# Performance work log

Measured on AMD Instinct MI355X. Metric: run time of the kernel, lower is better.

Reference implementation:

```python
import jax, jax.numpy as jnp
import numpy as np

V, E, H, B, S, T = 32000, 32, 128, 128, 512, 16


def _gru_cell(x, h, w_ih, w_hh, b_ih, b_hh):
    # PyTorch GRU cell semantics.  x: [B, in], h: [B, H]
    gi = x @ w_ih.T + b_ih              # [B, 3H]
    gh = h @ w_hh.T + b_hh              # [B, 3H]
    i_r, i_z, i_n = jnp.split(gi, 3, axis=-1)
    h_r, h_z, h_n = jnp.split(gh, 3, axis=-1)
    r = jax.nn.sigmoid(i_r + h_r)
    z = jax.nn.sigmoid(i_z + h_z)
    n = jnp.tanh(i_n + r * h_n)
    return (1.0 - z) * n + z * h


def setup_inputs() -> dict:
    key = jax.random.key(0)
    ks = jax.random.split(key, 24)
    Hh = H // 2  # encoder hidden per direction = 64
    u = lambda k, shp, fan: jax.random.uniform(k, shp, jnp.float32, -1.0, 1.0) / np.sqrt(fan)
    inp = {
        'inputs': jax.random.randint(ks[0], (B, S), 0, V),
        'targets': jax.random.randint(ks[1], (B, T), 0, V),
        'emb': jax.random.normal(ks[2], (V, E), jnp.float32),
        # encoder forward direction
        'W_ih_f': u(ks[3], (3 * Hh, E), Hh), 'W_hh_f': u(ks[4], (3 * Hh, Hh), Hh),
        'b_ih_f': u(ks[5], (3 * Hh,), Hh), 'b_hh_f': u(ks[6], (3 * Hh,), Hh),
        # encoder backward direction
        'W_ih_b': u(ks[7], (3 * Hh, E), Hh), 'W_hh_b': u(ks[8], (3 * Hh, Hh), Hh),
        'b_ih_b': u(ks[9], (3 * Hh,), Hh), 'b_hh_b': u(ks[10], (3 * Hh,), Hh),
        # sGate linears
        'W1': u(ks[11], (H, H), H), 'b1': u(ks[12], (H,), H),
        'W2': u(ks[13], (H, H), H), 'b2': u(ks[14], (H,), H),
        # decoder GRU (input E + H = 160, hidden H)
        'W_ih_d': u(ks[15], (3 * H, E + H), H), 'W_hh_d': u(ks[16], (3 * H, H), H),
        'b_ih_d': u(ks[17], (3 * H,), H), 'b_hh_d': u(ks[18], (3 * H,), H),
        # decoder2vocab
        'W_out': u(ks[19], (V, H), H), 'b_out': u(ks[20], (V,), H),
    }
    return inp


def reference(inputs, targets, emb, W_ih_f, W_hh_f, b_ih_f, b_hh_f,
              W_ih_b, W_hh_b, b_ih_b, b_hh_b, W1, b1, W2, b2,
              W_ih_d, W_hh_d, b_ih_d, b_hh_d, W_out, b_out):
    Hh = H // 2
    # ---- encode ----
    embeds = emb[inputs]                       # [B, S, E]
    xs = embeds.transpose(1, 0, 2)             # [S, B, E] time-major
    h0 = jnp.zeros((inputs.shape[0], Hh), jnp.float32)

    def fwd_step(h, x):
        h = _gru_cell(x, h, W_ih_f, W_hh_f, b_ih_f, b_hh_f)
        return h, h

    def bwd_step(h, x):
        h = _gru_cell(x, h, W_ih_b, W_hh_b, b_ih_b, b_hh_b)
        return h, h

    h_f, outs_f = jax.lax.scan(fwd_step, h0, xs)
    h_b, outs_b = jax.lax.scan(bwd_step, h0, xs[::-1])
    outs_b = outs_b[::-1]
    outputs = jnp.concatenate([outs_f, outs_b], axis=-1).transpose(1, 0, 2)  # [B, S, H]
    sn = jnp.concatenate([h_f, h_b], axis=-1)[:, None, :]                    # [B, 1, H]
    sGate = jax.nn.sigmoid(outputs @ W1.T + b1 + sn @ W2.T + b2)
    enc_outs = outputs * sGate                                               # [B, S, H]

    # ---- attention decode (teacher forcing) ----
    h_dec0 = sn[:, 0, :]                       # [B, H]
    words = targets[:, :-1].T                  # [T-1, B]

    def dec_step(h, w):
        e = emb[w]                                                  # [B, E]
        alpha = jax.nn.softmax(jnp.einsum('bd,bsd->bs', h, enc_outs))
        c_t = jnp.einsum('bs,bsd->bd', alpha, enc_outs)             # [B, H]
        h = _gru_cell(jnp.concatenate([c_t, e], axis=-1), h,
                      W_ih_d, W_hh_d, b_ih_d, b_hh_d)
        return h, h @ W_out.T + b_out

    _, logits = jax.lax.scan(dec_step, h_dec0, words)  # [T-1, B, V]
    return logits.transpose(1, 0, 2)                   # [B, T-1, V]
```

## Files before the change

kernel.cpp:

```cpp
#include <hip/hip_runtime.h>
#include <hip/hip_bf16.h>


typedef unsigned short u16;
typedef unsigned int u32;
typedef __attribute__((ext_vector_type(8))) short short8;
typedef __attribute__((ext_vector_type(4))) float f32x4;

#define V_ 32000
#define E_ 32
#define H_ 128
#define B_ 128
#define S_ 512
#define TDEC 15

__device__ __forceinline__ float bfu(u32 u) {
    union { u32 i; float f; } v; v.i = u << 16; return v.f;
}
__device__ __forceinline__ u16 f2bf(float f) {
    union { float f; u32 i; } v; v.f = f;
    u32 x = v.i;
    u32 r = (x + 0x7fffu + ((x >> 16) & 1u)) >> 16;
    return (u16)r;
}
__device__ __forceinline__ void bf8_to_f(const uint4 p, float* f) {
    f[0] = bfu(p.x & 0xffffu); f[1] = bfu(p.x >> 16);
    f[2] = bfu(p.y & 0xffffu); f[3] = bfu(p.y >> 16);
    f[4] = bfu(p.z & 0xffffu); f[5] = bfu(p.z >> 16);
    f[6] = bfu(p.w & 0xffffu); f[7] = bfu(p.w >> 16);
}
__device__ __forceinline__ float sigm_fast(float x) { return 1.f / (1.f + __expf(-x)); }
__device__ __forceinline__ float tanh_fast(float x) {
    const float t = __expf(2.f * x);
    return (t - 1.f) / (t + 1.f);
}

__global__ __launch_bounds__(384) void gi_kernel(
    const int* __restrict__ inputs, const float* __restrict__ emb,
    const float* __restrict__ Wih_f, const float* __restrict__ bih_f,
    const float* __restrict__ bhh_f,
    const float* __restrict__ Wih_b, const float* __restrict__ bih_b,
    const float* __restrict__ bhh_b,
    float* __restrict__ gi)
{
    const int b  = blockIdx.x >> 3;
    const int s0 = (blockIdx.x & 7) << 6;
    const int tid = threadIdx.x;

    __shared__ float xs[64][E_];
    __shared__ int idx[64];
    if (tid < 64) idx[tid] = inputs[b * S_ + s0 + tid];
    __syncthreads();
    for (int i = tid; i < 64 * E_; i += 384) {
        xs[i >> 5][i & 31] = emb[(unsigned)idx[i >> 5] * E_ + (i & 31)];
    }
    __syncthreads();

    const int dir = (tid >= 192) ? 1 : 0;
    const int j = tid - dir * 192;
    const float* Wih = dir ? Wih_b : Wih_f;
    const float* bih = dir ? bih_b : bih_f;
    const float* bhh = dir ? bhh_b : bhh_f;

    float w[E_];
    #pragma unroll
    for (int k = 0; k < E_; k += 4)
        *(float4*)(w + k) = *(const float4*)(Wih + j * E_ + k);
    const float c = bih[j] + (j < 128 ? bhh[j] : 0.f);

    float* gout = gi + (((size_t)(dir * B_ + b)) * S_ + s0) * 192 + j;
    for (int r = 0; r < 64; r++) {
        const float4* xr = (const float4*)xs[r];
        float a0 = 0.f, a1 = 0.f, a2 = 0.f, a3 = 0.f;
        #pragma unroll
        for (int q = 0; q < E_ / 4; q++) {
            const float4 x = xr[q];
            a0 += x.x * w[4 * q + 0]; a1 += x.y * w[4 * q + 1];
            a2 += x.z * w[4 * q + 2]; a3 += x.w * w[4 * q + 3];
        }
        gout[(size_t)r * 192] = ((a0 + a1) + (a2 + a3)) + c;
    }
}

__global__ __launch_bounds__(192, 1) void encoder_kernel(
    const float* __restrict__ gi,
    const float* __restrict__ Whh_f, const float* __restrict__ bhh_f,
    const float* __restrict__ Whh_b, const float* __restrict__ bhh_b,
    u16* __restrict__ outputs, float* __restrict__ sn)
{
    const int tid = threadIdx.x;
    const int g = tid >> 6;
    const int j = tid & 63;
    const int b = blockIdx.x & 127;
    const int dir = blockIdx.x >> 7;

    const float* Whh = dir ? Whh_b : Whh_f;
    const float* bhh = dir ? bhh_b : bhh_f;

    f32x4 wv[16];
    {
        const f32x4* wr = (const f32x4*)(Whh + (g * 64 + j) * 64);
        #pragma unroll
        for (int k = 0; k < 16; k++) wv[k] = wr[k];
    }
    const float badd = (g == 2) ? bhh[128 + j] : 0.f;

    __shared__ __attribute__((aligned(16))) float hs[64];
    __shared__ float sg[4 * 64];
    if (tid < 64) hs[tid] = 0.f;
    float hmine = 0.f;

    const float* gp = gi + ((size_t)(dir * B_ + b)) * S_ * 192 + g * 64 + j;
    u16* orow = outputs + ((size_t)b * S_) * H_ + (dir << 6) + j;

    const int st = dir ? -1 : 1;
    int oc = dir ? (S_ - 1) : 0;

    float pa = gp[(long)oc * 192];
    float pb = gp[(long)(oc + st) * 192];

#define ENC_STEP(PCUR)                                                         \
    {                                                                          \
        __syncthreads();                  \
        f32x4 acc = {0.f, 0.f, 0.f, 0.f};                                      \
        _Pragma("unroll")                                                      \
        for (int q = 0; q < 16; q++)                                           \
            acc += *(const f32x4*)(hs + 4 * q) * wv[q];                        \
        const float d = (acc[0] + acc[1]) + (acc[2] + acc[3]);                 \
        if (g == 2) { sg[128 + j] = d + badd; sg[192 + j] = PCUR; }            \
        else        { sg[g * 64 + j] = d + PCUR; }                             \
        PCUR = gp[(long)(oc + 2 * st) * 192];           \
        __syncthreads();                                         \
        if (g == 0) {                                                          \
            const float r = sigm_fast(sg[j]);                                  \
            const float z = sigm_fast(sg[64 + j]);                             \
            const float n = tanh_fast(sg[192 + j] + r * sg[128 + j]);          \
            const float hn = n + z * (hmine - n);                              \
            hmine = hn;                                                        \
            hs[j] = hn;                                                        \
            orow[(long)oc * H_] = f2bf(hn);                                    \
        }                                                                      \
        oc += st;                                                              \
    }

    for (int s = 0; s < S_; s += 2) {
        ENC_STEP(pa)
        ENC_STEP(pb)
    }
#undef ENC_STEP

    if (g == 0) sn[(b << 7) + (dir << 6) + j] = hmine;
}

__global__ __launch_bounds__(128) void t2_kernel(
    const float* __restrict__ sn, const float* __restrict__ W2,
    const float* __restrict__ b2, float* __restrict__ t2)
{
    const int b = blockIdx.x, h = threadIdx.x;
    __shared__ float s_[H_];
    s_[h] = sn[b * H_ + h];
    __syncthreads();
    const float4* wr = (const float4*)(W2 + h * H_);
    float a0 = 0.f, a1 = 0.f, a2 = 0.f, a3 = 0.f;
    #pragma unroll 4
    for (int k = 0; k < H_ / 4; k++) {
        const float4 p = wr[k];
        a0 += s_[4 * k + 0] * p.x; a1 += s_[4 * k + 1] * p.y;
        a2 += s_[4 * k + 2] * p.z; a3 += s_[4 * k + 3] * p.w;
    }
    t2[b * H_ + h] = ((a0 + a1) + (a2 + a3)) + b2[h];
}

__global__ __launch_bounds__(256) void cvt_bf16_kernel(
    const float* __restrict__ src, u16* __restrict__ dst)
{
    const int i = (blockIdx.x * 256 + threadIdx.x) * 4;
    const float4 p = *(const float4*)(src + i);
    ushort4 q;
    q.x = f2bf(p.x); q.y = f2bf(p.y); q.z = f2bf(p.z); q.w = f2bf(p.w);
    *(ushort4*)(dst + i) = q;
}

__global__ __launch_bounds__(256) void gate_mfma_kernel(
    const u16* __restrict__ outputs, const u16* __restrict__ W1b,
    const float* __restrict__ b1, const float* __restrict__ t2,
    u16* __restrict__ enc)
{
    const int l = threadIdx.x & 63;
    const int w = threadIdx.x >> 6;
    const int tile_m = blockIdx.x * 64 + w * 16;
    const int row_a = tile_m + (l & 15);
    const int kb = (l >> 4) * 8;
    const int b = blockIdx.x >> 3;

    f32x4 acc[8] = {};
    #pragma unroll
    for (int kk = 0; kk < 4; kk++) {
        const int k0 = kk * 32 + kb;
        const short8 af = *(const short8*)(outputs + row_a * H_ + k0);
        #pragma unroll
        for (int i = 0; i < 8; i++) {
            const int n = i * 16 + (l & 15);
            const short8 bv = *(const short8*)(W1b + n * H_ + k0);
            acc[i] = __builtin_amdgcn_mfma_f32_16x16x32_bf16(af, bv, acc[i], 0, 0, 0);
        }
    }

    const int m_base = tile_m + (l >> 4) * 4;
    #pragma unroll
    for (int i = 0; i < 8; i++) {
        const int n = i * 16 + (l & 15);
        const float bias = b1[n] + t2[b * H_ + n];
        #pragma unroll
        for (int r = 0; r < 4; r++) {
            const int m = m_base + r;
            const float g = sigm_fast(acc[i][r] + bias);
            const float o = bfu(outputs[m * H_ + n]);
            enc[m * H_ + n] = f2bf(o * g);
        }
    }
}

__global__ __launch_bounds__(512, 1) void decoder_kernel(
    const int* __restrict__ targets, const float* __restrict__ emb,
    const float* __restrict__ Wihd, const float* __restrict__ Whhd,
    const float* __restrict__ bihd, const float* __restrict__ bhhd,
    const u16* __restrict__ enc, const float* __restrict__ sn,
    u16* __restrict__ h_all)
{
    const int b = blockIdx.x;
    const int tid = threadIdx.x;
    const int lane = tid & 63;
    const int wid = tid >> 6;

    __shared__ __attribute__((aligned(16))) u16 enc_lds[S_ * H_];
    __shared__ __attribute__((aligned(16))) float xh[288];
    __shared__ float sc[S_];
    __shared__ float redm[8], reds[8];
    __shared__ __attribute__((aligned(16))) float cpart[32][H_];
    __shared__ float gf[256];
    __shared__ float gin[128], ghn[128];

    const u16* encb = enc + b * S_ * H_;

    {
        const int c = tid & 15;
        const int sb = tid >> 4;
        #pragma unroll
        for (int i = 0; i < 16; i++) {
            const int s = i * 32 + sb;
            const uint4 p = *(const uint4*)(encb + s * H_ + c * 8);
            *(uint4*)(enc_lds + s * H_ + ((c ^ (s & 15)) * 8)) = p;
        }
    }
    if (tid < H_) xh[160 + tid] = sn[b * H_ + tid];
    __syncthreads();

    for (int t = 0; t < TDEC; t++) {
        const int word = targets[b * 16 + t];

        float d;
        {
            const int s = tid;
            const int sx = s & 15;
            float a0 = 0.f, a1 = 0.f, a2 = 0.f, a3 = 0.f;
            #pragma unroll
            for (int c = 0; c < 16; c++) {
                const uint4 p = *(const uint4*)(enc_lds + s * H_ + ((c ^ sx) * 8));
                float f[8]; bf8_to_f(p, f);
                const f32x4 h0 = *(const f32x4*)(xh + 160 + c * 8);
                const f32x4 h1 = *(const f32x4*)(xh + 160 + c * 8 + 4);
                a0 += h0[0] * f[0]; a1 += h0[1] * f[1];
                a2 += h0[2] * f[2]; a3 += h0[3] * f[3];
                a0 += h1[0] * f[4]; a1 += h1[1] * f[5];
                a2 += h1[2] * f[6]; a3 += h1[3] * f[7];
            }
            d = (a0 + a1) + (a2 + a3);
        }

        float m = d;
        #pragma unroll
        for (int off = 32; off > 0; off >>= 1) m = fmaxf(m, __shfl_xor(m, off));
        if (lane == 0) redm[wid] = m;
        __syncthreads();
        float bm = redm[0];
        #pragma unroll
        for (int i = 1; i < 8; i++) bm = fmaxf(bm, redm[i]);
        const float e = __expf(d - bm);
        float ssum = e;
        #pragma unroll
        for (int off = 32; off > 0; off >>= 1) ssum += __shfl_xor(ssum, off);
        if (lane == 0) reds[wid] = ssum;
        __syncthreads();
        float tot = reds[0];
        #pragma unroll
        for (int i = 1; i < 8; i++) tot += reds[i];
        sc[tid] = e * (1.f / tot);
        __syncthreads();

        {
            const int c = tid & 15;
            const int q = tid >> 4;
            f32x4 ca = {0.f, 0.f, 0.f, 0.f}, cb = {0.f, 0.f, 0.f, 0.f};
            #pragma unroll
            for (int i = 0; i < 16; i++) {
                const int s = q * 16 + i;
                const float al = sc[s];
                const uint4 p = *(const uint4*)(enc_lds + s * H_ + ((c ^ i) * 8));
                float f[8]; bf8_to_f(p, f);
                ca[0] += al * f[0]; ca[1] += al * f[1];
                ca[2] += al * f[2]; ca[3] += al * f[3];
                cb[0] += al * f[4]; cb[1] += al * f[5];
                cb[2] += al * f[6]; cb[3] += al * f[7];
            }
            *(f32x4*)(cpart[q] + c * 8) = ca;
            *(f32x4*)(cpart[q] + c * 8 + 4) = cb;
        }
        __syncthreads();
        if (tid < H_) {
            float s0 = 0.f, s1 = 0.f, s2 = 0.f, s3 = 0.f;
            #pragma unroll
            for (int p = 0; p < 32; p += 4) {
                s0 += cpart[p + 0][tid]; s1 += cpart[p + 1][tid];
                s2 += cpart[p + 2][tid]; s3 += cpart[p + 3][tid];
            }
            xh[tid] = (s0 + s1) + (s2 + s3);
        } else if (tid < H_ + E_) xh[tid] = emb[(unsigned)word * E_ + (tid - H_)];
        __syncthreads();

        if (tid < 256) {
            const int j = tid;
            const float4* wr = (const float4*)(Wihd + j * (H_ + E_));
            const float4* xr = (const float4*)(xh);
            float g0 = 0.f, g1 = 0.f, g2 = 0.f, g3 = 0.f;
            #pragma unroll 8
            for (int k = 0; k < (H_ + E_) / 4; k++) {
                const float4 p = wr[k];
                const float4 x = xr[k];
                g0 += x.x * p.x; g1 += x.y * p.y; g2 += x.z * p.z; g3 += x.w * p.w;
            }
            const float4* hr = (const float4*)(Whhd + j * H_);
            const float4* xr2 = (const float4*)(xh + 160);
            #pragma unroll 8
            for (int k = 0; k < H_ / 4; k++) {
                const float4 p = hr[k];
                const float4 x = xr2[k];
                g0 += x.x * p.x; g1 += x.y * p.y; g2 += x.z * p.z; g3 += x.w * p.w;
            }
            gf[j] = ((g0 + g1) + (g2 + g3)) + (bihd[j] + bhhd[j]);
        } else if (tid < 384) {
            const int j = tid;
            const float4* wr = (const float4*)(Wihd + j * (H_ + E_));
            const float4* xr = (const float4*)(xh);
            float g0 = 0.f, g1 = 0.f, g2 = 0.f, g3 = 0.f;
            #pragma unroll 8
            for (int k = 0; k < (H_ + E_) / 4; k++) {
                const float4 p = wr[k];
                const float4 x = xr[k];
                g0 += x.x * p.x; g1 += x.y * p.y; g2 += x.z * p.z; g3 += x.w * p.w;
            }
            gin[j - 256] = ((g0 + g1) + (g2 + g3)) + bihd[j];
        } else {
            const int j = tid - 128;
            const float4* hr = (const float4*)(Whhd + j * H_);
            const float4* xr2 = (const float4*)(xh + 160);
            float g0 = 0.f, g1 = 0.f, g2 = 0.f, g3 = 0.f;
            #pragma unroll 8
            for (int k = 0; k < H_ / 4; k++) {
                const float4 p = hr[k];
                const float4 x = xr2[k];
                g0 += x.x * p.x; g1 += x.y * p.y; g2 += x.z * p.z; g3 += x.w * p.w;
            }
            ghn[j - 256] = ((g0 + g1) + (g2 + g3)) + bhhd[j];
        }
        __syncthreads();

        if (tid < H_) {
            const float r = sigm_fast(gf[tid]);
            const float z = sigm_fast(gf[128 + tid]);
            const float n = tanh_fast(gin[tid] + r * ghn[tid]);
            const float hn = (1.f - z) * n + z * xh[160 + tid];
            xh[160 + tid] = hn;
            h_all[(t * B_ + b) * H_ + tid] = f2bf(hn);
        }
        __syncthreads();
    }
}

__global__ __launch_bounds__(256) void logits_kernel(
    const u16* __restrict__ hall, const u16* __restrict__ Woutb,
    const float* __restrict__ bout, float* __restrict__ out)
{
    const int l = threadIdx.x & 63;
    const int w = threadIdx.x >> 6;
    const int tile_n = blockIdx.x * 64;
    const int tile_m = blockIdx.y * 64 + w * 16;

    f32x4 acc[4] = {};
    const int row_a = tile_m + (l & 15);
    const int kb = (l >> 4) * 8;

    #pragma unroll
    for (int kk = 0; kk < 4; kk++) {
        const int k0 = kk * 32 + kb;
        const short8 af = *(const short8*)(hall + row_a * H_ + k0);
        #pragma unroll
        for (int i = 0; i < 4; i++) {
            const int n = tile_n + i * 16 + (l & 15);
            const short8 bv = *(const short8*)(Woutb + n * H_ + k0);
            acc[i] = __builtin_amdgcn_mfma_f32_16x16x32_bf16(af, bv, acc[i], 0, 0, 0);
        }
    }

    const int m_base = tile_m + (l >> 4) * 4;
    #pragma unroll
    for (int i = 0; i < 4; i++) {
        const int n = tile_n + i * 16 + (l & 15);
        const float bias = bout[n];
        #pragma unroll
        for (int r = 0; r < 4; r++) {
            const int m = m_base + r;
            const int t = m >> 7;
            const int bb = m & 127;
            out[(size_t)(bb * TDEC + t) * V_ + n] = acc[i][r] + bias;
        }
    }
}

extern "C" void kernel_launch(void* const* d_in, const int* in_sizes, int n_in,
                              void* d_out, int out_size, void* d_ws, size_t ws_size,
                              hipStream_t stream) {
    const int*   inputs  = (const int*)d_in[0];
    const int*   targets = (const int*)d_in[1];
    const float* emb     = (const float*)d_in[2];
    const float* Wih_f   = (const float*)d_in[3];
    const float* Whh_f   = (const float*)d_in[4];
    const float* bih_f   = (const float*)d_in[5];
    const float* bhh_f   = (const float*)d_in[6];
    const float* Wih_b   = (const float*)d_in[7];
    const float* Whh_b   = (const float*)d_in[8];
    const float* bih_b   = (const float*)d_in[9];
    const float* bhh_b   = (const float*)d_in[10];
    const float* W1      = (const float*)d_in[11];
    const float* b1      = (const float*)d_in[12];
    const float* W2      = (const float*)d_in[13];
    const float* b2      = (const float*)d_in[14];
    const float* Wihd    = (const float*)d_in[15];
    const float* Whhd    = (const float*)d_in[16];
    const float* bihd    = (const float*)d_in[17];
    const float* bhhd    = (const float*)d_in[18];
    const float* Wout    = (const float*)d_in[19];
    const float* bout    = (const float*)d_in[20];
    float* out = (float*)d_out;

    u16*   outputs = (u16*)d_out;
    u16*   enc     = (u16*)((char*)d_out + 16777216);
    u16*   W1b     = (u16*)((char*)d_out + 33554432);
    float* gi      = (float*)((char*)d_out + 33619968);

    char* ws = (char*)d_ws;
    float* sn    = (float*)(ws);
    float* t2    = (float*)(ws + 65536);
    u16*   h_all = (u16*)(ws + 131072);
    u16*   Woutb = (u16*)(ws + 622592);

    gi_kernel<<<B_ * (S_ / 64), 384, 0, stream>>>(inputs, emb, Wih_f, bih_f, bhh_f,
                                                  Wih_b, bih_b, bhh_b, gi);
    encoder_kernel<<<256, 192, 0, stream>>>(gi, Whh_f, bhh_f, Whh_b, bhh_b, outputs, sn);
    t2_kernel<<<128, 128, 0, stream>>>(sn, W2, b2, t2);
    cvt_bf16_kernel<<<H_ * H_ / 1024, 256, 0, stream>>>(W1, W1b);
    cvt_bf16_kernel<<<V_ * H_ / 1024, 256, 0, stream>>>(Wout, Woutb);
    gate_mfma_kernel<<<B_ * S_ / 64, 256, 0, stream>>>(outputs, W1b, b1, t2, enc);
    decoder_kernel<<<128, 512, 0, stream>>>(targets, emb, Wihd, Whhd, bihd, bhhd,
                                            enc, sn, h_all);
    logits_kernel<<<dim3(500, 30), 256, 0, stream>>>(h_all, Woutb, bout, out);
}
```

Before: 945.4 us.

## Double-buffer encoder gate scratch to drop a barrier; vectorize logits stores via LDS

The encoder GRU step now keeps the gate pre-activations in a double-buffered shared array, so one of the two __syncthreads per timestep can be removed. All warps compute the cell update redundantly and write hs, with only warp 0 writing the output row. The vocab projection epilogue stages the MFMA accumulators in LDS and writes float4 rows with the bias added, replacing scattered scalar stores. The redundant hs writes from several warps race benignly because they store identical values. Dropping the barrier relies on the double buffer to prevent read-after-write conflicts on sg.

```diff
diff --git a/kernel.cpp b/kernel.cpp
--- a/kernel.cpp
+++ b/kernel.cpp
@@ -106,8 +106,8 @@
     const float badd = (g == 2) ? bhh[128 + j] : 0.f;
 
     __shared__ __attribute__((aligned(16))) float hs[64];
-    __shared__ float sg[4 * 64];
-    if (tid < 64) hs[tid] = 0.f;
+    __shared__ float sg[2][4 * 64];
+    hs[j] = 0.f;
     float hmine = 0.f;
 
     const float* gp = gi + ((size_t)(dir * B_ + b)) * S_ * 192 + g * 64 + j;
@@ -119,33 +119,30 @@
     float pa = gp[(long)oc * 192];
     float pb = gp[(long)(oc + st) * 192];
 
-#define ENC_STEP(PCUR)                                                         \
+#define ENC_STEP(PCUR, BUF)                                                    \
     {                                                                          \
-        __syncthreads();                  \
         f32x4 acc = {0.f, 0.f, 0.f, 0.f};                                      \
         _Pragma("unroll")                                                      \
         for (int q = 0; q < 16; q++)                                           \
             acc += *(const f32x4*)(hs + 4 * q) * wv[q];                        \
         const float d = (acc[0] + acc[1]) + (acc[2] + acc[3]);                 \
-        if (g == 2) { sg[128 + j] = d + badd; sg[192 + j] = PCUR; }            \
-        else        { sg[g * 64 + j] = d + PCUR; }                             \
+        if (g == 2) { sg[BUF][128 + j] = d + badd; sg[BUF][192 + j] = PCUR; }  \
+        else        { sg[BUF][g * 64 + j] = d + PCUR; }                        \
         PCUR = gp[(long)(oc + 2 * st) * 192];           \
-        __syncthreads();                                         \
-        if (g == 0) {                                                          \
-            const float r = sigm_fast(sg[j]);                                  \
-            const float z = sigm_fast(sg[64 + j]);                             \
-            const float n = tanh_fast(sg[192 + j] + r * sg[128 + j]);          \
-            const float hn = n + z * (hmine - n);                              \
-            hmine = hn;                                                        \
-            hs[j] = hn;                                                        \
-            orow[(long)oc * H_] = f2bf(hn);                                    \
-        }                                                                      \
+        __syncthreads();                                 \
+        const float r = sigm_fast(sg[BUF][j]);                                 \
+        const float z = sigm_fast(sg[BUF][64 + j]);                            \
+        const float n = tanh_fast(sg[BUF][192 + j] + r * sg[BUF][128 + j]);    \
+        const float hn = n + z * (hmine - n);                                  \
+        hmine = hn;                                                            \
+        hs[j] = hn;                                 \
+        if (g == 0) orow[(long)oc * H_] = f2bf(hn);                            \
         oc += st;                                                              \
     }
 
     for (int s = 0; s < S_; s += 2) {
-        ENC_STEP(pa)
-        ENC_STEP(pb)
+        ENC_STEP(pa, 0)
+        ENC_STEP(pb, 1)
     }
 #undef ENC_STEP
 
@@ -412,18 +409,27 @@
         }
     }
 
-    const int m_base = tile_m + (l >> 4) * 4;
+    __shared__ __attribute__((aligned(16))) float ct[4][16][68];
+    const int rq = l >> 4;
+    const int c16 = l & 15;
     #pragma unroll
     for (int i = 0; i < 4; i++) {
-        const int n = tile_n + i * 16 + (l & 15);
-        const float bias = bout[n];
         #pragma unroll
         for (int r = 0; r < 4; r++) {
-            const int m = m_base + r;
-            const int t = m >> 7;
-            const int bb = m & 127;
-            out[(size_t)(bb * TDEC + t) * V_ + n] = acc[i][r] + bias;
-        }
+            ct[w][rq * 4 + r][i * 16 + c16] = acc[i][r];
+        }
+    }
+
+    float4 bi = *(const float4*)(bout + tile_n + c16 * 4);
+    #pragma unroll
+    for (int p = 0; p < 4; p++) {
+        const int rl = p * 4 + rq;
+        const int m = tile_m + rl;
+        const int t = m >> 7;
+        const int bb = m & 127;
+        float4 v = *(const float4*)(&ct[w][rl][c16 * 4]);
+        v.x += bi.x; v.y += bi.y; v.z += bi.z; v.w += bi.w;
+        *(float4*)(out + (size_t)(bb * TDEC + t) * V_ + tile_n + c16 * 4) = v;
     }
 }
 
```

After: 954.9 us. About the same (+1.0%).
